# Optimization experiments

Hardware: AMD Instinct MI355X
Metric: run time of the kernel (lower is better)

The kernel has to match this reference:

```python
import jax, jax.numpy as jnp
import numpy as np

B, S, D = 2, 2048, 1024
KQ_EMB, V_EMB, H = 1024, 1024, 16
KQ_HD, V_HD = KQ_EMB // H, V_EMB // H


def setup_inputs() -> dict:
    key = jax.random.key(0)
    ks = jax.random.split(key, 7)
    scale = 1.0 / np.sqrt(D)
    return {
        "q": jax.random.normal(ks[0], (B, S, D), dtype=jnp.float32),
        "k": jax.random.normal(ks[1], (B, S, D), dtype=jnp.float32),
        "v": jax.random.normal(ks[2], (B, S, D), dtype=jnp.float32),
        "Wq": jax.random.normal(ks[3], (D, KQ_EMB), dtype=jnp.float32) * scale,
        "Wk": jax.random.normal(ks[4], (D, KQ_EMB), dtype=jnp.float32) * scale,
        "Wv": jax.random.normal(ks[5], (D, V_EMB), dtype=jnp.float32) * scale,
        "Wo": jax.random.normal(ks[6], (V_EMB, V_EMB), dtype=jnp.float32) * (1.0 / np.sqrt(V_EMB)),
        "masked": 1,
    }


def reference(q, k, v, Wq, Wk, Wv, Wo, masked):
    Bq, Sq, _ = q.shape
    # projections (Linear, no bias)
    Q = (q @ Wq).reshape(Bq, Sq, H, KQ_HD).transpose(0, 2, 1, 3)  # [B,H,S,hd]
    K = (k @ Wk).reshape(Bq, Sq, H, KQ_HD).transpose(0, 2, 1, 3)
    V = (v @ Wv).reshape(Bq, Sq, H, V_HD).transpose(0, 2, 1, 3)
    scores = jnp.einsum("bhqd,bhkd->bhqk", Q, K) * (1.0 / KQ_HD ** 0.5)
    if masked:
        causal = jnp.tril(jnp.ones((Sq, Sq), dtype=bool))  # True = keep
        scores = jnp.where(causal, scores, jnp.float32(-jnp.inf))
    weights = jax.nn.softmax(scores, axis=-1)
    attn_out = jnp.einsum("bhqk,bhkd->bhqd", weights, V)  # [B,H,S,v_hd]
    merged = attn_out.transpose(0, 2, 1, 3).reshape(Bq, Sq, H * V_HD)
    output = merged @ Wo
    return output, attn_out
```

## Files before the change

### kernel.cpp

```cpp
#include <hip/hip_runtime.h>
#include <math.h>

constexpr int CB = 2, CS = 2048, CD = 1024, CH = 16, CHD = 64;
constexpr int CEMB = 1024;

typedef unsigned short ushort_t;
typedef __attribute__((ext_vector_type(8))) short short8;
typedef __attribute__((ext_vector_type(4))) float f32x4;

__device__ __forceinline__ ushort_t f2bf(float x) {
    unsigned int u = __builtin_bit_cast(unsigned int, x);
    u = u + 0x7fffu + ((u >> 16) & 1u);
    return (ushort_t)(u >> 16);
}
__device__ __forceinline__ float bf2f(ushort_t h) {
    unsigned int u = ((unsigned int)h) << 16;
    return __builtin_bit_cast(float, u);
}

__global__ __launch_bounds__(256) void convert_wt(
    const float* __restrict__ W0, const float* __restrict__ W1,
    const float* __restrict__ W2, const float* __restrict__ W3,
    ushort_t* __restrict__ H0, ushort_t* __restrict__ L0,
    ushort_t* __restrict__ H1, ushort_t* __restrict__ L1,
    ushort_t* __restrict__ H2, ushort_t* __restrict__ L2,
    ushort_t* __restrict__ H3, ushort_t* __restrict__ L3) {
    const float* W;
    ushort_t* Hd;
    ushort_t* Ld;
    switch (blockIdx.z) {
        case 0: W = W0; Hd = H0; Ld = L0; break;
        case 1: W = W1; Hd = H1; Ld = L1; break;
        case 2: W = W2; Hd = H2; Ld = L2; break;
        default: W = W3; Hd = H3; Ld = L3; break;
    }
    const int n0 = blockIdx.x * 64, k0 = blockIdx.y * 64;
    __shared__ float Ls[64][65];
    const int t = threadIdx.x;
#pragma unroll
    for (int rep = 0; rep < 4; rep++) {
        const int r = rep * 16 + (t >> 4);
        const int c4 = (t & 15) * 4;
        *(float4*)&Ls[r][c4] = *(const float4*)&W[(size_t)(k0 + r) * CEMB + n0 + c4];
    }
    __syncthreads();
    const int n = t >> 2, kc = (t & 3) * 16;
#pragma unroll
    for (int c = 0; c < 2; c++) {
        union { ushort_t us[8]; uint4 v; } H, L;
#pragma unroll
        for (int j = 0; j < 8; j++) {
            const float x = Ls[kc + c * 8 + j][n];
            const ushort_t h = f2bf(x);
            H.us[j] = h;
            L.us[j] = f2bf(x - bf2f(h));
        }
        const size_t dst = (size_t)(n0 + n) * CEMB + k0 + kc + c * 8;
        *(uint4*)&Hd[dst] = H.v;
        *(uint4*)&Ld[dst] = L.v;
    }
}

template <bool GATHER_A>
__device__ __forceinline__ void gemm_split_body(
    const float* __restrict__ A, const ushort_t* __restrict__ Bhi,
    const ushort_t* __restrict__ Blo, float* __restrict__ Cf,
    ushort_t* __restrict__ C0, ushort_t* __restrict__ C1, float scale,
    int emode, int M, int N, int K) {
    __shared__ ushort_t As_hi[128 * 32], As_lo[128 * 32];
    __shared__ ushort_t Bs_hi[128 * 32], Bs_lo[128 * 32];
    const int tid = threadIdx.x;
    const int row0 = blockIdx.y * 128, col0 = blockIdx.x * 128;
    const int w = tid >> 6, l = tid & 63, lr = l & 15, lg = l >> 4;
    const int wm = w >> 1, wn = w & 1;

    f32x4 acc[4][4];
#pragma unroll
    for (int i = 0; i < 4; i++)
#pragma unroll
        for (int j = 0; j < 4; j++) acc[i][j] = (f32x4)(0.f);

    const int st_r = tid >> 1;
    const int st_kh = (tid & 1) * 16;

    for (int k0 = 0; k0 < K; k0 += 32) {
        {
            const int gm = row0 + st_r;
            const int gk = k0 + st_kh;
            const float* src;
            if (GATHER_A) {
                const int b_ = gm >> 11, s_ = gm & 2047;
                const int h_ = gk >> 6, d_ = gk & 63;
                src = &A[(((size_t)b_ * CH + h_) * CS + s_) * CHD + d_];
            } else {
                src = &A[(size_t)gm * K + gk];
            }
            float va[16];
#pragma unroll
            for (int r = 0; r < 4; r++)
                *(float4*)&va[r * 4] = *(const float4*)&src[r * 4];
#pragma unroll
            for (int c = 0; c < 2; c++) {
                union { ushort_t us[8]; uint4 v; } H, L;
#pragma unroll
                for (int j = 0; j < 8; j++) {
                    const float x = va[c * 8 + j];
                    const ushort_t h = f2bf(x);
                    H.us[j] = h;
                    L.us[j] = f2bf(x - bf2f(h));
                }
                const int chunk = (st_kh >> 3) + c;
                const int csw = chunk ^ ((st_r >> 1) & 3);
                *(uint4*)&As_hi[st_r * 32 + csw * 8] = H.v;
                *(uint4*)&As_lo[st_r * 32 + csw * 8] = L.v;
            }
        }
        {
            const size_t base = (size_t)(col0 + st_r) * K + k0 + st_kh;
#pragma unroll
            for (int c = 0; c < 2; c++) {
                const uint4 hv = *(const uint4*)&Bhi[base + c * 8];
                const uint4 lv = *(const uint4*)&Blo[base + c * 8];
                const int chunk = (st_kh >> 3) + c;
                const int csw = chunk ^ ((st_r >> 1) & 3);
                *(uint4*)&Bs_hi[st_r * 32 + csw * 8] = hv;
                *(uint4*)&Bs_lo[st_r * 32 + csw * 8] = lv;
            }
        }
        __syncthreads();

        short8 ah[4], al[4], bh[4], bl[4];
#pragma unroll
        for (int i = 0; i < 4; i++) {
            const int r = wm * 64 + i * 16 + lr;
            const int cs = lg ^ ((r >> 1) & 3);
            ah[i] = *(const short8*)&As_hi[r * 32 + cs * 8];
            al[i] = *(const short8*)&As_lo[r * 32 + cs * 8];
        }
#pragma unroll
        for (int j = 0; j < 4; j++) {
            const int cc = wn * 64 + j * 16 + lr;
            const int cs = lg ^ ((cc >> 1) & 3);
            bh[j] = *(const short8*)&Bs_hi[cc * 32 + cs * 8];
            bl[j] = *(const short8*)&Bs_lo[cc * 32 + cs * 8];
        }
#pragma unroll
        for (int j = 0; j < 4; j++)
#pragma unroll
            for (int i = 0; i < 4; i++) {
                acc[i][j] = __builtin_amdgcn_mfma_f32_16x16x32_bf16(
                    al[i], bh[j], acc[i][j], 0, 0, 0);
                acc[i][j] = __builtin_amdgcn_mfma_f32_16x16x32_bf16(
                    ah[i], bl[j], acc[i][j], 0, 0, 0);
                acc[i][j] = __builtin_amdgcn_mfma_f32_16x16x32_bf16(
                    ah[i], bh[j], acc[i][j], 0, 0, 0);
            }
        __syncthreads();
    }

#pragma unroll
    for (int i = 0; i < 4; i++)
#pragma unroll
        for (int j = 0; j < 4; j++) {
            const int cc = col0 + wn * 64 + j * 16 + lr;
#pragma unroll
            for (int r = 0; r < 4; r++) {
                const int cr = row0 + wm * 64 + i * 16 + lg * 4 + r;
                const float vv = acc[i][j][r];
                if (emode == 0) {
                    Cf[(size_t)cr * N + cc] = vv;
                } else {
                    const int b_ = cr >> 11, s_ = cr & 2047;
                    const int h_ = cc >> 6, d_ = cc & 63;
                    if (emode == 1) {
                        const size_t idx =
                            (((size_t)b_ * CH + h_) * CS + s_) * CHD + d_;
                        const float x = vv * scale;
                        const ushort_t hb = f2bf(x);
                        C0[idx] = hb;
                        C1[idx] = f2bf(x - bf2f(hb));
                    } else {
                        C0[(((size_t)b_ * CH + h_) * CHD + d_) * CS + s_] =
                            f2bf(vv);
                    }
                }
            }
        }
}

__global__ __launch_bounds__(256, 2) void qkv_proj(
    const float* __restrict__ q, const float* __restrict__ k,
    const float* __restrict__ v,
    const ushort_t* __restrict__ hq, const ushort_t* __restrict__ lq,
    const ushort_t* __restrict__ hk, const ushort_t* __restrict__ lk,
    const ushort_t* __restrict__ hv, const ushort_t* __restrict__ lv,
    ushort_t* __restrict__ Qhi, ushort_t* __restrict__ Qlo,
    ushort_t* __restrict__ Khi, ushort_t* __restrict__ Klo,
    ushort_t* __restrict__ Vt) {
    const float* A;
    const ushort_t* Bh;
    const ushort_t* Bl;
    ushort_t* C0;
    ushort_t* C1 = nullptr;
    float scale = 1.0f;
    int emode;
    if (blockIdx.z == 0) {
        A = q; Bh = hq; Bl = lq; C0 = Qhi; C1 = Qlo; scale = 0.125f; emode = 1;
    } else if (blockIdx.z == 1) {
        A = k; Bh = hk; Bl = lk; C0 = Khi; C1 = Klo; emode = 1;
    } else {
        A = v; Bh = hv; Bl = lv; C0 = Vt; emode = 2;
    }
    gemm_split_body<false>(A, Bh, Bl, nullptr, C0, C1, scale, emode,
                           CB * CS, CEMB, CD);
}

__global__ __launch_bounds__(256, 2) void out_proj(
    const float* __restrict__ attn, const ushort_t* __restrict__ ho,
    const ushort_t* __restrict__ lo_, float* __restrict__ out) {
    gemm_split_body<true>(attn, ho, lo_, out, nullptr, nullptr, 1.0f, 0,
                          CB * CS, CEMB, CEMB);
}

constexpr int LP = 72;

__global__ __launch_bounds__(256, 2) void flash_mfma(
    const ushort_t* __restrict__ Qhi, const ushort_t* __restrict__ Qlo,
    const ushort_t* __restrict__ Khi, const ushort_t* __restrict__ Klo,
    const ushort_t* __restrict__ Vt, float* __restrict__ O,
    const int* __restrict__ maskedp) {
    __shared__ ushort_t Ks_hi[64 * LP];
    __shared__ ushort_t Ks_lo[64 * LP];
    __shared__ ushort_t Vs[64 * LP];
    __shared__ ushort_t Ps[4][32 * LP];
    const int tid = threadIdx.x;
    const int w = tid >> 6, l = tid & 63, lr = l & 15, lg = l >> 4;
    const int j = blockIdx.x;
    const int bh = blockIdx.y;
    const int masked = maskedp[0];
    const int myqt = (w < 2) ? (31 - j) : j;
    const int q0 = myqt * 64 + (w & 1) * 32;
    const size_t bhoff = (size_t)bh * CS * CHD;

    short8 qh[2][2], ql[2][2];
#pragma unroll
    for (int qf = 0; qf < 2; qf++)
#pragma unroll
        for (int ds = 0; ds < 2; ds++) {
            const size_t off = bhoff + (size_t)(q0 + qf * 16 + lr) * CHD +
                               ds * 32 + lg * 8;
            qh[qf][ds] = *(const short8*)&Qhi[off];
            ql[qf][ds] = *(const short8*)&Qlo[off];
        }

    f32x4 Oacc[2][4];
    float m_i[2], l_i[2];
#pragma unroll
    for (int qf = 0; qf < 2; qf++) {
        m_i[qf] = -INFINITY;
        l_i[qf] = 0.f;
#pragma unroll
        for (int d = 0; d < 4; d++) Oacc[qf][d] = (f32x4)(0.f);
    }

    const int tmax = masked ? (31 - j) : 31;
    const int tBmax = masked ? j : 31;

    const int st_r = tid >> 2;
    const int st_c = (tid & 3);

    uint4 pk_hi[2], pk_lo[2], pv[2];
#pragma unroll
    for (int p = 0; p < 2; p++) {
        const int c = st_c + p * 4;
        const size_t kgl = bhoff + (size_t)(0 * 64 + st_r) * CHD + c * 8;
        pk_hi[p] = *(const uint4*)&Khi[kgl];
        pk_lo[p] = *(const uint4*)&Klo[kgl];
        const size_t vgl = ((size_t)bh * CHD + st_r) * CS + 0 * 64 + c * 8;
        pv[p] = *(const uint4*)&Vt[vgl];
    }

    for (int t = 0; t <= tmax; t++) {
#pragma unroll
        for (int p = 0; p < 2; p++) {
            const int c = st_c + p * 4;
            *(uint4*)&Ks_hi[st_r * LP + c * 8] = pk_hi[p];
            *(uint4*)&Ks_lo[st_r * LP + c * 8] = pk_lo[p];
            *(uint4*)&Vs[st_r * LP + c * 8] = pv[p];
        }
        __syncthreads();

        if (t < tmax) {
#pragma unroll
            for (int p = 0; p < 2; p++) {
                const int c = st_c + p * 4;
                const size_t kgl =
                    bhoff + (size_t)((t + 1) * 64 + st_r) * CHD + c * 8;
                pk_hi[p] = *(const uint4*)&Khi[kgl];
                pk_lo[p] = *(const uint4*)&Klo[kgl];
                const size_t vgl =
                    ((size_t)bh * CHD + st_r) * CS + (t + 1) * 64 + c * 8;
                pv[p] = *(const uint4*)&Vt[vgl];
            }
        }

        const bool act = (w < 2) || (t <= tBmax);
        if (act) {
            f32x4 S[2][4];
#pragma unroll
            for (int qf = 0; qf < 2; qf++)
#pragma unroll
                for (int kf = 0; kf < 4; kf++) S[qf][kf] = (f32x4)(0.f);
#pragma unroll
            for (int ds = 0; ds < 2; ds++) {
                short8 kh[4], kl[4];
#pragma unroll
                for (int kf = 0; kf < 4; kf++) {
                    const int off = (kf * 16 + lr) * LP + ds * 32 + lg * 8;
                    kh[kf] = *(const short8*)&Ks_hi[off];
                    kl[kf] = *(const short8*)&Ks_lo[off];
                }
#pragma unroll
                for (int qf = 0; qf < 2; qf++)
#pragma unroll
                    for (int kf = 0; kf < 4; kf++) {
                        S[qf][kf] = __builtin_amdgcn_mfma_f32_16x16x32_bf16(
                            kh[kf], ql[qf][ds], S[qf][kf], 0, 0, 0);
                        S[qf][kf] = __builtin_amdgcn_mfma_f32_16x16x32_bf16(
                            kl[kf], qh[qf][ds], S[qf][kf], 0, 0, 0);
                        S[qf][kf] = __builtin_amdgcn_mfma_f32_16x16x32_bf16(
                            kh[kf], qh[qf][ds], S[qf][kf], 0, 0, 0);
                    }
            }

            if (masked && t == myqt) {
#pragma unroll
                for (int qf = 0; qf < 2; qf++) {
                    const int qg = q0 + qf * 16 + lr;
#pragma unroll
                    for (int kf = 0; kf < 4; kf++)
#pragma unroll
                        for (int r = 0; r < 4; r++) {
                            const int kg = t * 64 + kf * 16 + 4 * lg + r;
                            if (kg > qg) S[qf][kf][r] = -INFINITY;
                        }
                }
            }

#pragma unroll
            for (int qf = 0; qf < 2; qf++) {
                float mt = -INFINITY;
#pragma unroll
                for (int kf = 0; kf < 4; kf++)
#pragma unroll
                    for (int r = 0; r < 4; r++) mt = fmaxf(mt, S[qf][kf][r]);
                mt = fmaxf(mt, __shfl_xor(mt, 16));
                mt = fmaxf(mt, __shfl_xor(mt, 32));
                const float mn = fmaxf(m_i[qf], mt);
                const float corr = __expf(m_i[qf] - mn);
                float rs = 0.f;
#pragma unroll
                for (int kf = 0; kf < 4; kf++)
#pragma unroll
                    for (int r = 0; r < 4; r++) {
                        const float p = __expf(S[qf][kf][r] - mn);
                        S[qf][kf][r] = p;
                        rs += p;
                    }
                rs += __shfl_xor(rs, 16);
                rs += __shfl_xor(rs, 32);
                l_i[qf] = l_i[qf] * corr + rs;
                m_i[qf] = mn;
#pragma unroll
                for (int df = 0; df < 4; df++) Oacc[qf][df] *= corr;

#pragma unroll
                for (int kf = 0; kf < 4; kf++)
#pragma unroll
                    for (int r2 = 0; r2 < 2; r2++) {
                        const unsigned int pk =
                            (unsigned int)f2bf(S[qf][kf][2 * r2]) |
                            ((unsigned int)f2bf(S[qf][kf][2 * r2 + 1]) << 16);
                        *(unsigned int*)&Ps[w][(qf * 16 + lr) * LP + kf * 16 +
                                               4 * lg + 2 * r2] = pk;
                    }
            }

#pragma unroll
            for (int ks = 0; ks < 2; ks++) {
                short8 vb[4], pb[2];
#pragma unroll
                for (int df = 0; df < 4; df++)
                    vb[df] = *(const short8*)&Vs[(df * 16 + lr) * LP +
                                                 ks * 32 + lg * 8];
#pragma unroll
                for (int qf = 0; qf < 2; qf++)
                    pb[qf] = *(const short8*)&Ps[w][(qf * 16 + lr) * LP +
                                                    ks * 32 + lg * 8];
#pragma unroll
                for (int qf = 0; qf < 2; qf++)
#pragma unroll
                    for (int df = 0; df < 4; df++)
                        Oacc[qf][df] = __builtin_amdgcn_mfma_f32_16x16x32_bf16(
                            vb[df], pb[qf], Oacc[qf][df], 0, 0, 0);
            }
        }
        __syncthreads();
    }

#pragma unroll
    for (int qf = 0; qf < 2; qf++) {
        const float inv = 1.0f / l_i[qf];
        const int qg = q0 + qf * 16 + lr;
#pragma unroll
        for (int df = 0; df < 4; df++)
#pragma unroll
            for (int r = 0; r < 4; r++) {
                O[bhoff + (size_t)qg * CHD + df * 16 + 4 * lg + r] =
                    Oacc[qf][df][r] * inv;
            }
    }
}

extern "C" void kernel_launch(void* const* d_in, const int* in_sizes, int n_in,
                              void* d_out, int out_size, void* d_ws,
                              size_t ws_size, hipStream_t stream) {
    const float* q  = (const float*)d_in[0];
    const float* k  = (const float*)d_in[1];
    const float* v  = (const float*)d_in[2];
    const float* Wq = (const float*)d_in[3];
    const float* Wk = (const float*)d_in[4];
    const float* Wv = (const float*)d_in[5];
    const float* Wo = (const float*)d_in[6];
    const int* masked = (const int*)d_in[7];

    float* out  = (float*)d_out;
    float* attn = out + (size_t)CB * CS * CEMB;

    const size_t NE = (size_t)CB * CS * CEMB;
    ushort_t* wsb = (ushort_t*)d_ws;
    ushort_t* Qhi = wsb + 0 * NE;
    ushort_t* Qlo = wsb + 1 * NE;
    ushort_t* Khi = wsb + 2 * NE;
    ushort_t* Klo = wsb + 3 * NE;
    ushort_t* Vt  = wsb + 4 * NE;
    ushort_t* wb  = wsb + 5 * NE;
    const size_t WN = (size_t)CEMB * CEMB;
    ushort_t* hq = wb + 0 * WN;  ushort_t* lq = wb + 1 * WN;
    ushort_t* hk = wb + 2 * WN;  ushort_t* lk = wb + 3 * WN;
    ushort_t* hv = wb + 4 * WN;  ushort_t* lv = wb + 5 * WN;
    ushort_t* ho = wb + 6 * WN;  ushort_t* lo_ = wb + 7 * WN;

    const int M = CB * CS;
    dim3 blk(256);

    convert_wt<<<dim3(16, 16, 4), blk, 0, stream>>>(
        Wq, Wk, Wv, Wo, hq, lq, hk, lk, hv, lv, ho, lo_);

    qkv_proj<<<dim3(CEMB / 128, M / 128, 3), blk, 0, stream>>>(
        q, k, v, hq, lq, hk, lk, hv, lv, Qhi, Qlo, Khi, Klo, Vt);

    flash_mfma<<<dim3(16, CB * CH), blk, 0, stream>>>(
        Qhi, Qlo, Khi, Klo, Vt, attn, masked);

    out_proj<<<dim3(CEMB / 128, M / 128), blk, 0, stream>>>(attn, ho, lo_, out);
}
```

Baseline: 378.7 us.

## Restructure flash attention to one Q tile per block and stage transposed stores

Flash attention now launches one 64-row query tile per block (1024 blocks, 16 rows per wave) instead of pairing long and short tiles in one block. Blocks are ordered longest-first and swizzled across bh, with launch bounds raised to 4 blocks per CU. The output and the V-transpose epilogue in the projection GEMM now stage results through shared memory, so global writes become vectorized and coalesced instead of scattered scalar stores. This adds more blocks and reloads of K/V per block, and gives up the per-block causal load balancing of the paired scheme.

```diff
diff --git a/kernel.cpp b/kernel.cpp
--- a/kernel.cpp
+++ b/kernel.cpp
@@ -61,14 +61,19 @@
     }
 }
 
+constexpr int LP = 72;
+
 template <bool GATHER_A>
 __device__ __forceinline__ void gemm_split_body(
     const float* __restrict__ A, const ushort_t* __restrict__ Bhi,
     const ushort_t* __restrict__ Blo, float* __restrict__ Cf,
     ushort_t* __restrict__ C0, ushort_t* __restrict__ C1, float scale,
     int emode, int M, int N, int K) {
-    __shared__ ushort_t As_hi[128 * 32], As_lo[128 * 32];
-    __shared__ ushort_t Bs_hi[128 * 32], Bs_lo[128 * 32];
+    __shared__ char gpool[36864];
+    ushort_t* const As_hi = (ushort_t*)gpool;
+    ushort_t* const As_lo = As_hi + 128 * 32;
+    ushort_t* const Bs_hi = As_lo + 128 * 32;
+    ushort_t* const Bs_lo = Bs_hi + 128 * 32;
     const int tid = threadIdx.x;
     const int row0 = blockIdx.y * 128, col0 = blockIdx.x * 128;
     const int w = tid >> 6, l = tid & 63, lr = l & 15, lg = l >> 4;
@@ -158,6 +163,35 @@
         __syncthreads();
     }
 
+    if (emode == 2) {
+        ushort_t* const T = (ushort_t*)gpool + w * 64 * LP;
+#pragma unroll
+        for (int i = 0; i < 4; i++)
+#pragma unroll
+            for (int j = 0; j < 4; j++) {
+                const unsigned int a =
+                    (unsigned int)f2bf(acc[i][j][0]) |
+                    ((unsigned int)f2bf(acc[i][j][1]) << 16);
+                const unsigned int b =
+                    (unsigned int)f2bf(acc[i][j][2]) |
+                    ((unsigned int)f2bf(acc[i][j][3]) << 16);
+                *(uint2*)&T[(j * 16 + lr) * LP + i * 16 + 4 * lg] =
+                    make_uint2(a, b);
+            }
+#pragma unroll
+        for (int grp = 0; grp < 8; grp++) {
+            const int dl = (l >> 3) + grp * 8;
+            const int s8 = (l & 7) * 8;
+            const uint4 vv = *(const uint4*)&T[dl * LP + s8];
+            const int gm = row0 + wm * 64 + s8;
+            const int b_ = gm >> 11, ss = gm & 2047;
+            const int dg = col0 + wn * 64 + dl;
+            const int h_ = dg >> 6, hd = dg & 63;
+            *(uint4*)&C0[(((size_t)b_ * CH + h_) * CHD + hd) * CS + ss] = vv;
+        }
+        return;
+    }
+
 #pragma unroll
     for (int i = 0; i < 4; i++)
 #pragma unroll
@@ -172,17 +206,12 @@
                 } else {
                     const int b_ = cr >> 11, s_ = cr & 2047;
                     const int h_ = cc >> 6, d_ = cc & 63;
-                    if (emode == 1) {
-                        const size_t idx =
-                            (((size_t)b_ * CH + h_) * CS + s_) * CHD + d_;
-                        const float x = vv * scale;
-                        const ushort_t hb = f2bf(x);
-                        C0[idx] = hb;
-                        C1[idx] = f2bf(x - bf2f(hb));
-                    } else {
-                        C0[(((size_t)b_ * CH + h_) * CHD + d_) * CS + s_] =
-                            f2bf(vv);
-                    }
+                    const size_t idx =
+                        (((size_t)b_ * CH + h_) * CS + s_) * CHD + d_;
+                    const float x = vv * scale;
+                    const ushort_t hb = f2bf(x);
+                    C0[idx] = hb;
+                    C1[idx] = f2bf(x - bf2f(hb));
                 }
             }
         }
@@ -222,61 +251,53 @@
                           CB * CS, CEMB, CEMB);
 }
 
-constexpr int LP = 72;
-
-__global__ __launch_bounds__(256, 2) void flash_mfma(
+__global__ __launch_bounds__(256, 4) void flash_mfma(
     const ushort_t* __restrict__ Qhi, const ushort_t* __restrict__ Qlo,
     const ushort_t* __restrict__ Khi, const ushort_t* __restrict__ Klo,
     const ushort_t* __restrict__ Vt, float* __restrict__ O,
     const int* __restrict__ maskedp) {
-    __shared__ ushort_t Ks_hi[64 * LP];
-    __shared__ ushort_t Ks_lo[64 * LP];
-    __shared__ ushort_t Vs[64 * LP];
-    __shared__ ushort_t Ps[4][32 * LP];
+    __shared__ char pool_raw[36864];
+    ushort_t* const Ks_hi = (ushort_t*)pool_raw;
+    ushort_t* const Ks_lo = Ks_hi + 64 * LP;
+    ushort_t* const Vs = Ks_lo + 64 * LP;
+    ushort_t* const PsA = Vs + 64 * LP;
+
     const int tid = threadIdx.x;
     const int w = tid >> 6, l = tid & 63, lr = l & 15, lg = l >> 4;
-    const int j = blockIdx.x;
-    const int bh = blockIdx.y;
     const int masked = maskedp[0];
-    const int myqt = (w < 2) ? (31 - j) : j;
-    const int q0 = myqt * 64 + (w & 1) * 32;
+    const int id = blockIdx.x;
+    const int sid = (id & 7) * 128 + (id >> 3);
+    const int bh = sid >> 5;
+    const int qt = 31 - (sid & 31);
+    const int q0 = qt * 64 + w * 16;
     const size_t bhoff = (size_t)bh * CS * CHD;
-
-    short8 qh[2][2], ql[2][2];
-#pragma unroll
-    for (int qf = 0; qf < 2; qf++)
-#pragma unroll
-        for (int ds = 0; ds < 2; ds++) {
-            const size_t off = bhoff + (size_t)(q0 + qf * 16 + lr) * CHD +
-                               ds * 32 + lg * 8;
-            qh[qf][ds] = *(const short8*)&Qhi[off];
-            ql[qf][ds] = *(const short8*)&Qlo[off];
-        }
-
-    f32x4 Oacc[2][4];
-    float m_i[2], l_i[2];
-#pragma unroll
-    for (int qf = 0; qf < 2; qf++) {
-        m_i[qf] = -INFINITY;
-        l_i[qf] = 0.f;
-#pragma unroll
-        for (int d = 0; d < 4; d++) Oacc[qf][d] = (f32x4)(0.f);
-    }
-
-    const int tmax = masked ? (31 - j) : 31;
-    const int tBmax = masked ? j : 31;
-
+    ushort_t* const Ps = PsA + w * 16 * LP;
+
+    short8 qh[2], ql[2];
+#pragma unroll
+    for (int ds = 0; ds < 2; ds++) {
+        const size_t off = bhoff + (size_t)(q0 + lr) * CHD + ds * 32 + lg * 8;
+        qh[ds] = *(const short8*)&Qhi[off];
+        ql[ds] = *(const short8*)&Qlo[off];
+    }
+
+    f32x4 Oacc[4];
+    float m_i = -INFINITY, l_i = 0.f;
+#pragma unroll
+    for (int df = 0; df < 4; df++) Oacc[df] = (f32x4)(0.f);
+
+    const int tmax = masked ? qt : 31;
     const int st_r = tid >> 2;
-    const int st_c = (tid & 3);
+    const int st_c = tid & 3;
 
     uint4 pk_hi[2], pk_lo[2], pv[2];
 #pragma unroll
     for (int p = 0; p < 2; p++) {
         const int c = st_c + p * 4;
-        const size_t kgl = bhoff + (size_t)(0 * 64 + st_r) * CHD + c * 8;
+        const size_t kgl = bhoff + (size_t)st_r * CHD + c * 8;
         pk_hi[p] = *(const uint4*)&Khi[kgl];
         pk_lo[p] = *(const uint4*)&Klo[kgl];
-        const size_t vgl = ((size_t)bh * CHD + st_r) * CS + 0 * 64 + c * 8;
+        const size_t vgl = ((size_t)bh * CHD + st_r) * CS + c * 8;
         pv[p] = *(const uint4*)&Vt[vgl];
     }
 
@@ -304,121 +325,105 @@
             }
         }
 
-        const bool act = (w < 2) || (t <= tBmax);
-        if (act) {
-            f32x4 S[2][4];
-#pragma unroll
-            for (int qf = 0; qf < 2; qf++)
-#pragma unroll
-                for (int kf = 0; kf < 4; kf++) S[qf][kf] = (f32x4)(0.f);
-#pragma unroll
-            for (int ds = 0; ds < 2; ds++) {
-                short8 kh[4], kl[4];
-#pragma unroll
-                for (int kf = 0; kf < 4; kf++) {
-                    const int off = (kf * 16 + lr) * LP + ds * 32 + lg * 8;
-                    kh[kf] = *(const short8*)&Ks_hi[off];
-                    kl[kf] = *(const short8*)&Ks_lo[off];
+        f32x4 S[4];
+#pragma unroll
+        for (int kf = 0; kf < 4; kf++) S[kf] = (f32x4)(0.f);
+#pragma unroll
+        for (int ds = 0; ds < 2; ds++) {
+            short8 kh[4], kl[4];
+#pragma unroll
+            for (int kf = 0; kf < 4; kf++) {
+                const int off = (kf * 16 + lr) * LP + ds * 32 + lg * 8;
+                kh[kf] = *(const short8*)&Ks_hi[off];
+                kl[kf] = *(const short8*)&Ks_lo[off];
+            }
+#pragma unroll
+            for (int kf = 0; kf < 4; kf++) {
+                S[kf] = __builtin_amdgcn_mfma_f32_16x16x32_bf16(
+                    kh[kf], ql[ds], S[kf], 0, 0, 0);
+                S[kf] = __builtin_amdgcn_mfma_f32_16x16x32_bf16(
+                    kl[kf], qh[ds], S[kf], 0, 0, 0);
+                S[kf] = __builtin_amdgcn_mfma_f32_16x16x32_bf16(
+                    kh[kf], qh[ds], S[kf], 0, 0, 0);
+            }
+        }
+
+        if (masked && t == qt) {
+            const int qg = q0 + lr;
+#pragma unroll
+            for (int kf = 0; kf < 4; kf++)
+#pragma unroll
+                for (int r = 0; r < 4; r++) {
+                    const int kg = t * 64 + kf * 16 + 4 * lg + r;
+                    if (kg > qg) S[kf][r] = -INFINITY;
                 }
-#pragma unroll
-                for (int qf = 0; qf < 2; qf++)
-#pragma unroll
-                    for (int kf = 0; kf < 4; kf++) {
-                        S[qf][kf] = __builtin_amdgcn_mfma_f32_16x16x32_bf16(
-                            kh[kf], ql[qf][ds], S[qf][kf], 0, 0, 0);
-                        S[qf][kf] = __builtin_amdgcn_mfma_f32_16x16x32_bf16(
-                            kl[kf], qh[qf][ds], S[qf][kf], 0, 0, 0);
-                        S[qf][kf] = __builtin_amdgcn_mfma_f32_16x16x32_bf16(
-                            kh[kf], qh[qf][ds], S[qf][kf], 0, 0, 0);
-                    }
-            }
-
-            if (masked && t == myqt) {
-#pragma unroll
-                for (int qf = 0; qf < 2; qf++) {
-                    const int qg = q0 + qf * 16 + lr;
-#pragma unroll
-                    for (int kf = 0; kf < 4; kf++)
-#pragma unroll
-                        for (int r = 0; r < 4; r++) {
-                            const int kg = t * 64 + kf * 16 + 4 * lg + r;
-                            if (kg > qg) S[qf][kf][r] = -INFINITY;
-                        }
+        }
+
+        {
+            float mt = -INFINITY;
+#pragma unroll
+            for (int kf = 0; kf < 4; kf++)
+#pragma unroll
+                for (int r = 0; r < 4; r++) mt = fmaxf(mt, S[kf][r]);
+            mt = fmaxf(mt, __shfl_xor(mt, 16));
+            mt = fmaxf(mt, __shfl_xor(mt, 32));
+            const float mn = fmaxf(m_i, mt);
+            const float corr = __expf(m_i - mn);
+            float rs = 0.f;
+#pragma unroll
+            for (int kf = 0; kf < 4; kf++)
+#pragma unroll
+                for (int r = 0; r < 4; r++) {
+                    const float p = __expf(S[kf][r] - mn);
+                    S[kf][r] = p;
+                    rs += p;
                 }
-            }
-
-#pragma unroll
-            for (int qf = 0; qf < 2; qf++) {
-                float mt = -INFINITY;
-#pragma unroll
-                for (int kf = 0; kf < 4; kf++)
-#pragma unroll
-                    for (int r = 0; r < 4; r++) mt = fmaxf(mt, S[qf][kf][r]);
-                mt = fmaxf(mt, __shfl_xor(mt, 16));
-                mt = fmaxf(mt, __shfl_xor(mt, 32));
-                const float mn = fmaxf(m_i[qf], mt);
-                const float corr = __expf(m_i[qf] - mn);
-                float rs = 0.f;
-#pragma unroll
-                for (int kf = 0; kf < 4; kf++)
-#pragma unroll
-                    for (int r = 0; r < 4; r++) {
-                        const float p = __expf(S[qf][kf][r] - mn);
-                        S[qf][kf][r] = p;
-                        rs += p;
-                    }
-                rs += __shfl_xor(rs, 16);
-                rs += __shfl_xor(rs, 32);
-                l_i[qf] = l_i[qf] * corr + rs;
-                m_i[qf] = mn;
-#pragma unroll
-                for (int df = 0; df < 4; df++) Oacc[qf][df] *= corr;
-
-#pragma unroll
-                for (int kf = 0; kf < 4; kf++)
-#pragma unroll
-                    for (int r2 = 0; r2 < 2; r2++) {
-                        const unsigned int pk =
-                            (unsigned int)f2bf(S[qf][kf][2 * r2]) |
-                            ((unsigned int)f2bf(S[qf][kf][2 * r2 + 1]) << 16);
-                        *(unsigned int*)&Ps[w][(qf * 16 + lr) * LP + kf * 16 +
-                                               4 * lg + 2 * r2] = pk;
-                    }
-            }
-
-#pragma unroll
-            for (int ks = 0; ks < 2; ks++) {
-                short8 vb[4], pb[2];
-#pragma unroll
-                for (int df = 0; df < 4; df++)
-                    vb[df] = *(const short8*)&Vs[(df * 16 + lr) * LP +
-                                                 ks * 32 + lg * 8];
-#pragma unroll
-                for (int qf = 0; qf < 2; qf++)
-                    pb[qf] = *(const short8*)&Ps[w][(qf * 16 + lr) * LP +
-                                                    ks * 32 + lg * 8];
-#pragma unroll
-                for (int qf = 0; qf < 2; qf++)
-#pragma unroll
-                    for (int df = 0; df < 4; df++)
-                        Oacc[qf][df] = __builtin_amdgcn_mfma_f32_16x16x32_bf16(
-                            vb[df], pb[qf], Oacc[qf][df], 0, 0, 0);
-            }
+            rs += __shfl_xor(rs, 16);
+            rs += __shfl_xor(rs, 32);
+            l_i = l_i * corr + rs;
+            m_i = mn;
+#pragma unroll
+            for (int df = 0; df < 4; df++) Oacc[df] *= corr;
+        }
+
+#pragma unroll
+        for (int kf = 0; kf < 4; kf++) {
+            const unsigned int a = (unsigned int)f2bf(S[kf][0]) |
+                                   ((unsigned int)f2bf(S[kf][1]) << 16);
+            const unsigned int b = (unsigned int)f2bf(S[kf][2]) |
+                                   ((unsigned int)f2bf(S[kf][3]) << 16);
+            *(uint2*)&Ps[lr * LP + kf * 16 + 4 * lg] = make_uint2(a, b);
+        }
+
+#pragma unroll
+        for (int ks = 0; ks < 2; ks++) {
+            short8 vb[4];
+#pragma unroll
+            for (int df = 0; df < 4; df++)
+                vb[df] = *(const short8*)&Vs[(df * 16 + lr) * LP + ks * 32 +
+                                             lg * 8];
+            const short8 pb =
+                *(const short8*)&Ps[lr * LP + ks * 32 + lg * 8];
+#pragma unroll
+            for (int df = 0; df < 4; df++)
+                Oacc[df] = __builtin_amdgcn_mfma_f32_16x16x32_bf16(
+                    vb[df], pb, Oacc[df], 0, 0, 0);
         }
         __syncthreads();
     }
 
-#pragma unroll
-    for (int qf = 0; qf < 2; qf++) {
-        const float inv = 1.0f / l_i[qf];
-        const int qg = q0 + qf * 16 + lr;
-#pragma unroll
-        for (int df = 0; df < 4; df++)
-#pragma unroll
-            for (int r = 0; r < 4; r++) {
-                O[bhoff + (size_t)qg * CHD + df * 16 + 4 * lg + r] =
-                    Oacc[qf][df][r] * inv;
-            }
+    float* const T = (float*)pool_raw + (size_t)w * 16 * LP;
+    const float inv = 1.0f / l_i;
+#pragma unroll
+    for (int df = 0; df < 4; df++) {
+        f32x4 vv = Oacc[df] * inv;
+        *(f32x4*)&T[lr * LP + df * 16 + 4 * lg] = vv;
+    }
+#pragma unroll
+    for (int grp = 0; grp < 4; grp++) {
+        const int qrow = grp * 4 + lg;
+        const float4 vv = *(const float4*)&T[qrow * LP + lr * 4];
+        *(float4*)&O[bhoff + (size_t)(q0 + qrow) * CHD + lr * 4] = vv;
     }
 }
 
@@ -460,7 +465,7 @@
     qkv_proj<<<dim3(CEMB / 128, M / 128, 3), blk, 0, stream>>>(
         q, k, v, hq, lq, hk, lk, hv, lv, Qhi, Qlo, Khi, Klo, Vt);
 
-    flash_mfma<<<dim3(16, CB * CH), blk, 0, stream>>>(
+    flash_mfma<<<dim3(32 * CB * CH), blk, 0, stream>>>(
         Qhi, Qlo, Khi, Klo, Vt, attn, masked);
 
     out_proj<<<dim3(CEMB / 128, M / 128), blk, 0, stream>>>(attn, ho, lo_, out);
```

After: 464.4 us. 22.6% more time.
